# Optimization experiments

Hardware: AMD Instinct MI355X
Metric: run time of the kernel (lower is better)

Reference implementation:

```python
import jax, jax.numpy as jnp
import numpy as np

B, N, F = 64, 128, 4
H = 100


def setup_inputs() -> dict:
    key = jax.random.key(0)
    ks = jax.random.split(key, 8)
    x = jax.random.normal(ks[0], (B, N, F), dtype=jnp.float32)
    in_hitnr = jax.random.randint(ks[1], (B, N), 0, N, dtype=jnp.int32)
    W1 = jax.random.normal(ks[2], (2 * F, H), dtype=jnp.float32) * (1.0 / np.sqrt(2 * F))
    b1 = jax.random.normal(ks[3], (H,), dtype=jnp.float32) * 0.01
    W2 = jax.random.normal(ks[4], (H, H), dtype=jnp.float32) * (1.0 / np.sqrt(H))
    b2 = jax.random.normal(ks[5], (H,), dtype=jnp.float32) * 0.01
    W3 = jax.random.normal(ks[6], (H, 1), dtype=jnp.float32) * (1.0 / np.sqrt(H))
    b3 = jax.random.normal(ks[7], (1,), dtype=jnp.float32) * 0.01
    return {"x": x, "in_hitnr": in_hitnr, "W1": W1, "b1": b1,
            "W2": W2, "b2": b2, "W3": W3, "b3": b3}


def reference(x, in_hitnr, W1, b1, W2, b2, W3, b3):
    n = x.shape[1]
    # itertools.combinations(range(n), 2) == lexicographic upper-triangle order
    i1, i2 = jnp.triu_indices(n, k=1)  # each [num_pairs]
    # pairwise gather + concat: [B, P, 2F]
    pairs = jnp.concatenate([x[:, i1], x[:, i2]], axis=-1)
    h = pairs @ W1 + b1                 # [B, P, 100]
    h = h @ W2 + b2                     # [B, P, 100]
    h = jax.nn.relu(h)                  # ReLU applied AFTER second linear (as in source)
    out = h @ W3 + b3                   # [B, P, 1]
    out = jax.nn.sigmoid(out)
    return jnp.squeeze(out, axis=-1)    # [B, P]
```

## Files before the change

kernel.cpp:

```cpp
#include <hip/hip_runtime.h>
#include <math.h>


namespace {
constexpr int B_    = 64;
constexpr int N_    = 128;
constexpr int F_    = 4;
constexpr int H_    = 100;
constexpr int TILE  = 32;
constexpr int NT    = N_ / TILE;
constexpr int NTP   = NT * (NT + 1) / 2;
constexpr int PAIRS = N_ * (N_ - 1) / 2;
constexpr int LDH   = H_ + 1;
}

__global__ __launch_bounds__(256)
void pairnet_fused(const float* __restrict__ x,
                   const float* __restrict__ W1,
                   const float* __restrict__ b1,
                   const float* __restrict__ W2,
                   const float* __restrict__ b2,
                   const float* __restrict__ W3,
                   const float* __restrict__ b3,
                   float* __restrict__ out)
{
    __shared__ float A_s [F_][H_];
    __shared__ float Bm_s[F_][H_];
    __shared__ float c_s [H_];
    __shared__ float w3_s[H_];
    __shared__ float U_s[TILE][LDH];
    __shared__ float V_s[TILE][LDH];

    const int tid = threadIdx.x;
    const int blk = blockIdx.x;
    const int b   = blk / NTP;
    int rem = blk % NTP;
    int ti = 0;
    while (rem >= NT - ti) { rem -= NT - ti; ++ti; }
    const int tj = ti + rem;

    for (int idx = tid; idx < 2 * F_ * H_ + H_; idx += 256) {
        if (idx < 2 * F_ * H_) {
            const int r = idx / H_;
            const int h = idx - r * H_;
            const float* w1r = W1 + r * H_;
            float s = 0.f;
            #pragma unroll 4
            for (int j = 0; j < H_; ++j) s = fmaf(w1r[j], W2[j * H_ + h], s);
            if (r < F_) A_s[r][h] = s; else Bm_s[r - F_][h] = s;
        } else {
            const int h = idx - 2 * F_ * H_;
            float s = b2[h];
            #pragma unroll 4
            for (int j = 0; j < H_; ++j) s = fmaf(b1[j], W2[j * H_ + h], s);
            c_s[h] = s;
        }
    }
    if (tid < H_) w3_s[tid] = W3[tid];
    __syncthreads();

    const int i0 = ti * TILE, j0 = tj * TILE;
    for (int idx = tid; idx < TILE * H_; idx += 256) {
        const int r = idx / H_;
        const int h = idx - r * H_;
        const float4 xi = ((const float4*)x)[b * N_ + i0 + r];
        U_s[r][h] = c_s[h] + xi.x * A_s[0][h] + xi.y * A_s[1][h]
                           + xi.z * A_s[2][h] + xi.w * A_s[3][h];
        const float4 xj = ((const float4*)x)[b * N_ + j0 + r];
        V_s[r][h] =        xj.x * Bm_s[0][h] + xj.y * Bm_s[1][h]
                         + xj.z * Bm_s[2][h] + xj.w * Bm_s[3][h];
    }
    __syncthreads();

    const int i2 = tid >> 4;
    const int j2 = tid & 15;
    const int ia = 2 * i2, ja = 2 * j2;
    float a00 = 0.f, a01 = 0.f, a10 = 0.f, a11 = 0.f;
    for (int h = 0; h < H_; ++h) {
        const float w  = w3_s[h];
        const float u0 = U_s[ia][h],     u1 = U_s[ia + 1][h];
        const float v0 = V_s[ja][h],     v1 = V_s[ja + 1][h];
        a00 = fmaf(w, fmaxf(u0 + v0, 0.f), a00);
        a01 = fmaf(w, fmaxf(u0 + v1, 0.f), a01);
        a10 = fmaf(w, fmaxf(u1 + v0, 0.f), a10);
        a11 = fmaf(w, fmaxf(u1 + v1, 0.f), a11);
    }
    const float b3v = b3[0];
    float* outb = out + b * PAIRS;
    const float accs[2][2] = {{a00, a01}, {a10, a11}};
    #pragma unroll
    for (int da = 0; da < 2; ++da) {
        #pragma unroll
        for (int dc = 0; dc < 2; ++dc) {
            const int gi = i0 + ia + da;
            const int gj = j0 + ja + dc;
            if (gi < gj) {
                const int p = (gi * (2 * N_ - gi - 1)) / 2 + (gj - gi - 1);
                const float z = accs[da][dc] + b3v;
                outb[p] = 1.f / (1.f + expf(-z));
            }
        }
    }
}

extern "C" void kernel_launch(void* const* d_in, const int* in_sizes, int n_in,
                              void* d_out, int out_size, void* d_ws, size_t ws_size,
                              hipStream_t stream) {
    const float* x  = (const float*)d_in[0];
    const float* W1 = (const float*)d_in[2];
    const float* b1 = (const float*)d_in[3];
    const float* W2 = (const float*)d_in[4];
    const float* b2 = (const float*)d_in[5];
    const float* W3 = (const float*)d_in[6];
    const float* b3 = (const float*)d_in[7];
    float* out = (float*)d_out;

    pairnet_fused<<<dim3(B_ * NTP), dim3(256), 0, stream>>>(
        x, W1, b1, W2, b2, W3, b3, out);
}
```

Before: 101.6 us.

## Hoist weight folding into a separate kernel and shrink pair tiles

Moves the W1·W2 and b1·W2+b2 folding out of every block into a small prologue kernel that writes a global buffer, so each of the many main blocks no longer redoes the roughly 90k-FMA fold. The main kernel switches to 16-wide tiles with 64 threads per block, interleaves the hidden dimension in shared memory so U/V can be read as float4, and uses the fast __expf. This adds a second kernel launch and a dependency through global memory, and computes more redundant tiles on the diagonal.

```diff
diff --git a/kernel.cpp b/kernel.cpp
--- a/kernel.cpp
+++ b/kernel.cpp
@@ -5,87 +5,99 @@
 namespace {
 constexpr int B_    = 64;
 constexpr int N_    = 128;
-constexpr int F_    = 4;
 constexpr int H_    = 100;
-constexpr int TILE  = 32;
+constexpr int TILE  = 16;
 constexpr int NT    = N_ / TILE;
 constexpr int NTP   = NT * (NT + 1) / 2;
 constexpr int PAIRS = N_ * (N_ - 1) / 2;
-constexpr int LDH   = H_ + 1;
+constexpr int FOLD_AB = 0;
+constexpr int FOLD_C  = 800;
+constexpr int FOLD_W3 = 900;
+constexpr int FOLD_B3 = 1000;
 }
 
+__device__ float g_fold[1001];
+
 __global__ __launch_bounds__(256)
-void pairnet_fused(const float* __restrict__ x,
-                   const float* __restrict__ W1,
-                   const float* __restrict__ b1,
-                   const float* __restrict__ W2,
-                   const float* __restrict__ b2,
-                   const float* __restrict__ W3,
-                   const float* __restrict__ b3,
-                   float* __restrict__ out)
+void fold_weights(const float* __restrict__ W1, const float* __restrict__ b1,
+                  const float* __restrict__ W2, const float* __restrict__ b2,
+                  const float* __restrict__ W3, const float* __restrict__ b3)
 {
-    __shared__ float A_s [F_][H_];
-    __shared__ float Bm_s[F_][H_];
-    __shared__ float c_s [H_];
+    const int idx = blockIdx.x * 256 + threadIdx.x;
+    if (idx < 800) {
+        const int r = idx / H_;
+        const int h = idx - r * H_;
+        const float* w1r = W1 + r * H_;
+        float s = 0.f;
+        #pragma unroll 5
+        for (int j = 0; j < H_; ++j) s = fmaf(w1r[j], W2[j * H_ + h], s);
+        g_fold[FOLD_AB + idx] = s;
+    } else if (idx < 900) {
+        const int h = idx - 800;
+        float s = b2[h];
+        #pragma unroll 5
+        for (int j = 0; j < H_; ++j) s = fmaf(b1[j], W2[j * H_ + h], s);
+        g_fold[FOLD_C + h] = s;
+    } else if (idx < 1000) {
+        g_fold[FOLD_W3 + (idx - 900)] = W3[idx - 900];
+    } else if (idx == 1000) {
+        g_fold[FOLD_B3] = b3[0];
+    }
+}
+
+__global__ __launch_bounds__(64)
+void pairnet_main(const float* __restrict__ x, float* __restrict__ out)
+{
+    __shared__ float U_s[50 * 2 * TILE];
+    __shared__ float V_s[50 * 2 * TILE];
     __shared__ float w3_s[H_];
-    __shared__ float U_s[TILE][LDH];
-    __shared__ float V_s[TILE][LDH];
 
     const int tid = threadIdx.x;
     const int blk = blockIdx.x;
     const int b   = blk / NTP;
-    int rem = blk % NTP;
+    int rem = blk - b * NTP;
     int ti = 0;
     while (rem >= NT - ti) { rem -= NT - ti; ++ti; }
     const int tj = ti + rem;
+    const int i0 = ti * TILE, j0 = tj * TILE;
 
-    for (int idx = tid; idx < 2 * F_ * H_ + H_; idx += 256) {
-        if (idx < 2 * F_ * H_) {
-            const int r = idx / H_;
-            const int h = idx - r * H_;
-            const float* w1r = W1 + r * H_;
-            float s = 0.f;
-            #pragma unroll 4
-            for (int j = 0; j < H_; ++j) s = fmaf(w1r[j], W2[j * H_ + h], s);
-            if (r < F_) A_s[r][h] = s; else Bm_s[r - F_][h] = s;
-        } else {
-            const int h = idx - 2 * F_ * H_;
-            float s = b2[h];
-            #pragma unroll 4
-            for (int j = 0; j < H_; ++j) s = fmaf(b1[j], W2[j * H_ + h], s);
-            c_s[h] = s;
-        }
-    }
-    if (tid < H_) w3_s[tid] = W3[tid];
-    __syncthreads();
+    for (int k = tid; k < H_; k += 64) w3_s[k] = g_fold[FOLD_W3 + k];
 
-    const int i0 = ti * TILE, j0 = tj * TILE;
-    for (int idx = tid; idx < TILE * H_; idx += 256) {
-        const int r = idx / H_;
-        const int h = idx - r * H_;
-        const float4 xi = ((const float4*)x)[b * N_ + i0 + r];
-        U_s[r][h] = c_s[h] + xi.x * A_s[0][h] + xi.y * A_s[1][h]
-                           + xi.z * A_s[2][h] + xi.w * A_s[3][h];
-        const float4 xj = ((const float4*)x)[b * N_ + j0 + r];
-        V_s[r][h] =        xj.x * Bm_s[0][h] + xj.y * Bm_s[1][h]
-                         + xj.z * Bm_s[2][h] + xj.w * Bm_s[3][h];
+    const float4* x4 = (const float4*)x;
+    for (int idx = tid; idx < TILE * H_; idx += 64) {
+        const int r = idx & (TILE - 1);
+        const int h = idx >> 4;
+        const int a = (h >> 1) * (2 * TILE) + r * 2 + (h & 1);
+        const float4 xi = x4[b * N_ + i0 + r];
+        U_s[a] = g_fold[FOLD_C + h]
+               + xi.x * g_fold[FOLD_AB + 0 * H_ + h]
+               + xi.y * g_fold[FOLD_AB + 1 * H_ + h]
+               + xi.z * g_fold[FOLD_AB + 2 * H_ + h]
+               + xi.w * g_fold[FOLD_AB + 3 * H_ + h];
+        const float4 xj = x4[b * N_ + j0 + r];
+        V_s[a] = xj.x * g_fold[FOLD_AB + 4 * H_ + h]
+               + xj.y * g_fold[FOLD_AB + 5 * H_ + h]
+               + xj.z * g_fold[FOLD_AB + 6 * H_ + h]
+               + xj.w * g_fold[FOLD_AB + 7 * H_ + h];
     }
     __syncthreads();
 
-    const int i2 = tid >> 4;
-    const int j2 = tid & 15;
+    const int i2 = tid >> 3;
+    const int j2 = tid & 7;
     const int ia = 2 * i2, ja = 2 * j2;
     float a00 = 0.f, a01 = 0.f, a10 = 0.f, a11 = 0.f;
-    for (int h = 0; h < H_; ++h) {
-        const float w  = w3_s[h];
-        const float u0 = U_s[ia][h],     u1 = U_s[ia + 1][h];
-        const float v0 = V_s[ja][h],     v1 = V_s[ja + 1][h];
-        a00 = fmaf(w, fmaxf(u0 + v0, 0.f), a00);
-        a01 = fmaf(w, fmaxf(u0 + v1, 0.f), a01);
-        a10 = fmaf(w, fmaxf(u1 + v0, 0.f), a10);
-        a11 = fmaf(w, fmaxf(u1 + v1, 0.f), a11);
+    #pragma unroll 2
+    for (int h2 = 0; h2 < 50; ++h2) {
+        const float2 w = *(const float2*)&w3_s[2 * h2];
+        const float4 u = *(const float4*)&U_s[h2 * 32 + ia * 2];
+        const float4 v = *(const float4*)&V_s[h2 * 32 + ja * 2];
+        a00 = fmaf(w.x, fmaxf(u.x + v.x, 0.f), fmaf(w.y, fmaxf(u.y + v.y, 0.f), a00));
+        a01 = fmaf(w.x, fmaxf(u.x + v.z, 0.f), fmaf(w.y, fmaxf(u.y + v.w, 0.f), a01));
+        a10 = fmaf(w.x, fmaxf(u.z + v.x, 0.f), fmaf(w.y, fmaxf(u.w + v.y, 0.f), a10));
+        a11 = fmaf(w.x, fmaxf(u.z + v.z, 0.f), fmaf(w.y, fmaxf(u.w + v.w, 0.f), a11));
     }
-    const float b3v = b3[0];
+
+    const float b3v = g_fold[FOLD_B3];
     float* outb = out + b * PAIRS;
     const float accs[2][2] = {{a00, a01}, {a10, a11}};
     #pragma unroll
@@ -97,7 +109,7 @@
             if (gi < gj) {
                 const int p = (gi * (2 * N_ - gi - 1)) / 2 + (gj - gi - 1);
                 const float z = accs[da][dc] + b3v;
-                outb[p] = 1.f / (1.f + expf(-z));
+                outb[p] = 1.f / (1.f + __expf(-z));
             }
         }
     }
@@ -115,6 +127,6 @@
     const float* b3 = (const float*)d_in[7];
     float* out = (float*)d_out;
 
-    pairnet_fused<<<dim3(B_ * NTP), dim3(256), 0, stream>>>(
-        x, W1, b1, W2, b2, W3, b3, out);
+    fold_weights<<<dim3(4), dim3(256), 0, stream>>>(W1, b1, W2, b2, W3, b3);
+    pairnet_main<<<dim3(B_ * NTP), dim3(64), 0, stream>>>(x, out);
 }
```

Measured after the change: 89.23 us. 1.14x faster.
